# Optimization experiments

Measured on AMD Instinct MI355X. Metric: run time of the kernel, lower is better.

## Reference

```python
import jax, jax.numpy as jnp
import numpy as np

N, E = 50000, 800000
IN_C, OUT_C, H, EW_DIM = 64, 32, 4, 16
NEG_SLOPE = 0.2


def setup_inputs() -> dict:
    key = jax.random.key(0)
    ks = jax.random.split(key, 10)
    x = jax.random.normal(ks[0], (N, IN_C), dtype=jnp.float32)
    src = jax.random.randint(ks[1], (E,), 0, N)
    dst = jax.random.randint(ks[2], (E,), 0, N)
    edge_index = jnp.stack([src, dst]).astype(jnp.int64)
    edge_weight = jax.random.normal(ks[3], (E, EW_DIM), dtype=jnp.float32)
    # GATConv params: lin weight [IN_C, H*OUT_C], bias [H*OUT_C], att_src/att_dst [H, OUT_C]
    s = 1.0 / np.sqrt(IN_C)
    W = jax.random.uniform(ks[4], (IN_C, H * OUT_C), minval=-s, maxval=s, dtype=jnp.float32)
    b = jnp.zeros((H * OUT_C,), dtype=jnp.float32)
    att_src = jax.random.normal(ks[5], (H, OUT_C), dtype=jnp.float32) * 0.1
    att_dst = jax.random.normal(ks[6], (H, OUT_C), dtype=jnp.float32) * 0.1
    # edge_weight_lin params: [EW_DIM, H], [H]
    se = 1.0 / np.sqrt(EW_DIM)
    Wl = jax.random.uniform(ks[7], (EW_DIM, H), minval=-se, maxval=se, dtype=jnp.float32)
    bl = jax.random.uniform(ks[8], (H,), minval=-se, maxval=se, dtype=jnp.float32)
    return {"x": x, "edge_index": edge_index, "edge_weight": edge_weight,
            "W": W, "b": b, "att_src": att_src, "att_dst": att_dst,
            "Wl": Wl, "bl": bl}


def gate_forward(x, edge_index, edge_weight, W, b, att_src, att_dst, Wl, bl):
    n = x.shape[0]
    h = (x @ W).reshape(n, H, OUT_C)                      # [N,H,C]
    a_src = jnp.einsum('nhc,hc->nh', h, att_src)          # [N,H]
    a_dst = jnp.einsum('nhc,hc->nh', h, att_dst)          # [N,H]
    # per-edge attention logits from edge weights (softmax over heads)
    edge_alpha = jax.nn.softmax(edge_weight @ Wl + bl, axis=1)  # [E,H]
    # add self loops (GATConv default add_self_loops=True, fill_value='mean')
    loop = jnp.arange(n)
    src = jnp.concatenate([edge_index[0], loop])
    dst = jnp.concatenate([edge_index[1], loop])
    loop_alpha = jnp.broadcast_to(edge_alpha.mean(axis=0), (n, H))
    ea = jnp.concatenate([edge_alpha, loop_alpha], axis=0)      # [E+N,H]
    # per-edge logits: gather src/dst contributions + edge term
    alpha = jax.nn.leaky_relu(a_src[src] + a_dst[dst] + ea, NEG_SLOPE)  # [E+N,H]
    # segment softmax grouped by destination node
    amax = jax.ops.segment_max(alpha, dst, num_segments=n)
    ex = jnp.exp(alpha - amax[dst])
    denom = jax.ops.segment_sum(ex, dst, num_segments=n)
    alpha = ex / (denom[dst] + 1e-16)                     # [E+N,H]
    # weighted messages, scatter-add aggregate
    msg = h[src] * alpha[:, :, None]                      # [E+N,H,C]
    out = jax.ops.segment_sum(msg, dst, num_segments=n)   # [N,H,C]
    return out.reshape(n, H * OUT_C) + b


def reference(x, edge_index, edge_weight, W, b, att_src, att_dst, Wl, bl):
    return gate_forward(x, edge_index, edge_weight, W, b, att_src, att_dst, Wl, bl)
```

## Files before the change

### kernel.cpp

```cpp
#include <hip/hip_runtime.h>
#include <math.h>

#define IN_C 64
#define HC 128
#define NHEAD 4
#define EWD 16
#define NEG 0.2f

__device__ __forceinline__ float lrelu(float v) { return v > 0.f ? v : NEG * v; }
__device__ __forceinline__ unsigned short f2b(float f) {
    unsigned int u = __float_as_uint(f);
    unsigned int r = ((u >> 16) & 1u) + 0x7fffu;
    return (unsigned short)((u + r) >> 16);
}
__device__ __forceinline__ float b2f(unsigned int lo16) {
    return __uint_as_float(lo16 << 16);
}

__global__ void k_feat(const float* __restrict__ x, const float* __restrict__ W,
                       const float* __restrict__ att_s, const float* __restrict__ att_d,
                       unsigned short* __restrict__ h_bf, float* __restrict__ a_src,
                       float* __restrict__ a_dst, int N) {
    __shared__ float Ws[IN_C * HC];
    __shared__ float xs[4][IN_C];
    const int tid = threadIdx.x;
    {
        const float4* W4 = (const float4*)W;
        float4* Ws4 = (float4*)Ws;
#pragma unroll
        for (int i = 0; i < (IN_C * HC / 4) / 128; ++i)
            Ws4[tid + i * 128] = W4[tid + i * 128];
    }
    const float as = att_s[tid];
    const float ad = att_d[tid];
    const int head = tid >> 5;
    for (int base = blockIdx.x * 4; base < N; base += gridDim.x * 4) {
        const int nrows = min(4, N - base);
        __syncthreads();
        if (tid < 64) {
            int r = tid >> 4, q = tid & 15;
            if (r < nrows)
                ((float4*)&xs[r][0])[q] = ((const float4*)(x + (size_t)(base + r) * IN_C))[q];
        }
        __syncthreads();
        for (int r = 0; r < nrows; ++r) {
            float acc = 0.f;
#pragma unroll
            for (int c = 0; c < IN_C; ++c)
                acc = fmaf(xs[r][c], Ws[c * HC + tid], acc);
            const int n = base + r;
            h_bf[(size_t)n * HC + tid] = f2b(acc);
            float ps = acc * as, pd = acc * ad;
#pragma unroll
            for (int off = 16; off; off >>= 1) {
                ps += __shfl_xor(ps, off, 32);
                pd += __shfl_xor(pd, off, 32);
            }
            if ((tid & 31) == 0) {
                a_src[n * NHEAD + head] = ps;
                a_dst[n * NHEAD + head] = pd;
            }
        }
    }
}

__global__ void k_count(const int* __restrict__ dst, int* __restrict__ deg, int E) {
    int e = blockIdx.x * 256 + threadIdx.x;
    if (e < E) atomicAdd(&deg[dst[e]], 1);
}

__global__ void k_scan1(const int* __restrict__ deg, int* __restrict__ part, int N) {
    const int b = blockIdx.x, tid = threadIdx.x;
    int base = b * 1024 + tid * 4;
    int s = 0;
#pragma unroll
    for (int k = 0; k < 4; ++k) { int i = base + k; if (i < N) s += deg[i]; }
#pragma unroll
    for (int off = 32; off; off >>= 1) s += __shfl_xor(s, off, 64);
    __shared__ int ls[4];
    if ((tid & 63) == 0) ls[tid >> 6] = s;
    __syncthreads();
    if (tid == 0) part[b] = ls[0] + ls[1] + ls[2] + ls[3];
}

__global__ void k_scan2(int* part, int nb) {
    const int tid = threadIdx.x;
    int orig = (tid < nb) ? part[tid] : 0;
    int v = orig;
#pragma unroll
    for (int off = 1; off < 64; off <<= 1) {
        int t = __shfl_up(v, off, 64);
        if (tid >= off) v += t;
    }
    if (tid < nb) part[tid] = v - orig;
}

__global__ void k_scan3(const int* __restrict__ deg, const int* __restrict__ part,
                        int* __restrict__ rowptr, int* __restrict__ cursor, int N, int E) {
    const int b = blockIdx.x, tid = threadIdx.x;
    int base = b * 1024 + tid * 4;
    int d[4]; int s = 0;
#pragma unroll
    for (int k = 0; k < 4; ++k) { int i = base + k; d[k] = (i < N) ? deg[i] : 0; s += d[k]; }
    int v = s;
#pragma unroll
    for (int off = 1; off < 64; off <<= 1) {
        int t = __shfl_up(v, off, 64);
        if ((tid & 63) >= off) v += t;
    }
    __shared__ int wsum[4];
    if ((tid & 63) == 63) wsum[tid >> 6] = v;
    __syncthreads();
    int waveoff = 0;
    const int w = tid >> 6;
    for (int k = 0; k < w; ++k) waveoff += wsum[k];
    int excl = v - s + waveoff + part[b];
#pragma unroll
    for (int k = 0; k < 4; ++k) {
        int i = base + k;
        if (i < N) { rowptr[i] = excl; cursor[i] = excl; }
        excl += d[k];
    }
    if (b == 0 && tid == 0) rowptr[N] = E;
}

__global__ void k_fill(const int* __restrict__ src, const int* __restrict__ dst,
                       const float* __restrict__ ew, const float* __restrict__ Wl,
                       const float* __restrict__ bl,
                       const float* __restrict__ a_src, const float* __restrict__ a_dst,
                       int* __restrict__ cursor, uint4* __restrict__ csr,
                       float* __restrict__ partial, int E) {
    __shared__ float sW[EWD * NHEAD];
    __shared__ float sb[NHEAD];
    __shared__ float sred[4][4];
    const int tid = threadIdx.x;
    if (tid < EWD * NHEAD) sW[tid] = Wl[tid];
    if (tid < NHEAD) sb[tid] = bl[tid];
    __syncthreads();
    float loc[4] = {0.f, 0.f, 0.f, 0.f};
    const int e = blockIdx.x * 256 + tid;
    if (e < E) {
        const float4* w4 = (const float4*)(ew + (size_t)e * EWD);
        float v[4];
#pragma unroll
        for (int hh = 0; hh < 4; ++hh) v[hh] = sb[hh];
#pragma unroll
        for (int q = 0; q < 4; ++q) {
            float4 t = w4[q];
            float tv[4] = {t.x, t.y, t.z, t.w};
#pragma unroll
            for (int k = 0; k < 4; ++k)
#pragma unroll
                for (int hh = 0; hh < 4; ++hh)
                    v[hh] = fmaf(tv[k], sW[(q * 4 + k) * 4 + hh], v[hh]);
        }
        float m = fmaxf(fmaxf(v[0], v[1]), fmaxf(v[2], v[3]));
        float s = 0.f;
#pragma unroll
        for (int hh = 0; hh < 4; ++hh) { v[hh] = __expf(v[hh] - m); s += v[hh]; }
        float inv = 1.f / s;
#pragma unroll
        for (int hh = 0; hh < 4; ++hh) { v[hh] *= inv; loc[hh] += v[hh]; }
        const int sn = src[e], dn = dst[e];
        float4 as = ((const float4*)a_src)[sn];
        float4 ad = ((const float4*)a_dst)[dn];
        unsigned int e0 = f2b(__expf(lrelu(as.x + ad.x + v[0])));
        unsigned int e1 = f2b(__expf(lrelu(as.y + ad.y + v[1])));
        unsigned int e2 = f2b(__expf(lrelu(as.z + ad.z + v[2])));
        unsigned int e3 = f2b(__expf(lrelu(as.w + ad.w + v[3])));
        uint4 rec;
        rec.x = (unsigned int)sn;
        rec.y = e0 | (e1 << 16);
        rec.z = e2 | (e3 << 16);
        rec.w = 0u;
        int slot = atomicAdd(&cursor[dn], 1);
        csr[slot] = rec;
    }
    const int w = tid >> 6;
#pragma unroll
    for (int hh = 0; hh < 4; ++hh) {
        float v = loc[hh];
#pragma unroll
        for (int off = 32; off; off >>= 1) v += __shfl_xor(v, off, 64);
        if ((tid & 63) == 0) sred[w][hh] = v;
    }
    __syncthreads();
    if (tid < 4)
        partial[blockIdx.x * 4 + tid] =
            sred[0][tid] + sred[1][tid] + sred[2][tid] + sred[3][tid];
}

__global__ void k_red(const float* __restrict__ partial, float* __restrict__ asum, int nb) {
    const int tid = threadIdx.x;
    const int w = tid >> 6, lane = tid & 63;
    float s = 0.f;
    for (int b = lane; b < nb; b += 64) s += partial[b * 4 + w];
#pragma unroll
    for (int off = 32; off; off >>= 1) s += __shfl_xor(s, off, 64);
    if (lane == 0) asum[w] = s;
}

__global__ void k_agg(const unsigned short* __restrict__ h_bf, const int* __restrict__ rowptr,
                      const uint4* __restrict__ csr,
                      const float* __restrict__ a_src, const float* __restrict__ a_dst,
                      const float* __restrict__ asum, const float* __restrict__ bias,
                      float* __restrict__ out, int N, int E) {
    const int d = blockIdx.x;
    const int tid = threadIdx.x;
    const int head = tid >> 5;
    __shared__ int ssrc[32];
    __shared__ float sex[32][4];
    const int r0 = rowptr[d], r1 = rowptr[d + 1];
    float acc = 0.f, den = 0.f;
    for (int base = r0; base < r1; base += 32) {
        const int cnt = min(32, r1 - base);
        __syncthreads();
        if (tid < cnt) {
            uint4 rec = csr[base + tid];
            ssrc[tid] = (int)rec.x;
            sex[tid][0] = b2f(rec.y & 0xffffu);
            sex[tid][1] = b2f(rec.y >> 16);
            sex[tid][2] = b2f(rec.z & 0xffffu);
            sex[tid][3] = b2f(rec.z >> 16);
        }
        __syncthreads();
        int k = 0;
        for (; k + 4 <= cnt; k += 4) {
            const int s0 = ssrc[k], s1 = ssrc[k+1], s2 = ssrc[k+2], s3 = ssrc[k+3];
            const float e0 = sex[k][head], e1 = sex[k+1][head],
                        e2 = sex[k+2][head], e3 = sex[k+3][head];
            const float h0 = b2f(h_bf[(size_t)s0 * HC + tid]);
            const float h1 = b2f(h_bf[(size_t)s1 * HC + tid]);
            const float h2 = b2f(h_bf[(size_t)s2 * HC + tid]);
            const float h3 = b2f(h_bf[(size_t)s3 * HC + tid]);
            acc = fmaf(h0, e0, acc); den += e0;
            acc = fmaf(h1, e1, acc); den += e1;
            acc = fmaf(h2, e2, acc); den += e2;
            acc = fmaf(h3, e3, acc); den += e3;
        }
        for (; k < cnt; ++k) {
            const int s = ssrc[k];
            const float ex = sex[k][head];
            acc = fmaf(b2f(h_bf[(size_t)s * HC + tid]), ex, acc);
            den += ex;
        }
    }
    const float mean = asum[head] * (1.0f / (float)E);
    float l = lrelu(a_src[d * NHEAD + head] + a_dst[d * NHEAD + head] + mean);
    const float exl = __expf(l);
    acc = fmaf(b2f(h_bf[(size_t)d * HC + tid]), exl, acc);
    den += exl;
    out[(size_t)d * HC + tid] = acc / (den + 1e-16f) + bias[tid];
}

extern "C" void kernel_launch(void* const* d_in, const int* in_sizes, int n_in,
                              void* d_out, int out_size, void* d_ws, size_t ws_size,
                              hipStream_t stream) {
    const float* x     = (const float*)d_in[0];
    const int*   ei    = (const int*)d_in[1];
    const float* ew    = (const float*)d_in[2];
    const float* W     = (const float*)d_in[3];
    const float* bias  = (const float*)d_in[4];
    const float* att_s = (const float*)d_in[5];
    const float* att_d = (const float*)d_in[6];
    const float* Wl    = (const float*)d_in[7];
    const float* bl    = (const float*)d_in[8];
    const int N = in_sizes[0] / IN_C;
    const int E = in_sizes[1] / 2;
    const int* src = ei;
    const int* dst = ei + E;
    float* out = (float*)d_out;

    const int FILL_BLOCKS = (E + 255) / 256;

    float* ws = (float*)d_ws;
    size_t off = 0;
    unsigned short* h_bf = (unsigned short*)(ws + off); off += (size_t)N * HC / 2;
    float* a_src  = ws + off; off += (size_t)N * NHEAD;
    float* a_dst  = ws + off; off += (size_t)N * NHEAD;
    int*   deg    = (int*)(ws + off); off += N;
    float* asum   = ws + off; off += 4;
    int*   part   = (int*)(ws + off); off += 64;
    int*   rowptr = (int*)(ws + off); off += (size_t)N + 4;
    int*   cursor = (int*)(ws + off); off += N;
    uint4* csr    = (uint4*)(ws + off); off += (size_t)E * 4;
    float* partial= ws + off; off += (size_t)FILL_BLOCKS * 4;

    hipMemsetAsync(deg, 0, (size_t)N * 4, stream);

    k_feat<<<2048, 128, 0, stream>>>(x, W, att_s, att_d, h_bf, a_src, a_dst, N);
    k_count<<<(E + 255) / 256, 256, 0, stream>>>(dst, deg, E);
    const int nb = (N + 1023) / 1024;
    k_scan1<<<nb, 256, 0, stream>>>(deg, part, N);
    k_scan2<<<1, 64, 0, stream>>>(part, nb);
    k_scan3<<<nb, 256, 0, stream>>>(deg, part, rowptr, cursor, N, E);
    k_fill<<<FILL_BLOCKS, 256, 0, stream>>>(src, dst, ew, Wl, bl, a_src, a_dst,
                                            cursor, csr, partial, E);
    k_red<<<1, 256, 0, stream>>>(partial, asum, FILL_BLOCKS);
    k_agg<<<N, 128, 0, stream>>>(h_bf, rowptr, csr, a_src, a_dst,
                                 asum, bias, out, N, E);
}
```

Before: 300.8 us.

## Register-block feature GEMM, batch edges per thread, drop LDS staging in aggregation

k_feat now keeps W columns in registers and computes 8 rows per iteration instead of streaming W from shared memory row by row. k_count and k_fill each handle four edges per thread, issuing their gathers and atomics in batches to raise memory-level parallelism. k_agg reads CSR records directly from global memory, with no shared staging or barriers. The risks are higher register pressure from the 64-float wreg array and redundant per-thread CSR loads in k_agg.

```diff
diff --git a/kernel.cpp b/kernel.cpp
--- a/kernel.cpp
+++ b/kernel.cpp
@@ -16,57 +16,76 @@
 __device__ __forceinline__ float b2f(unsigned int lo16) {
     return __uint_as_float(lo16 << 16);
 }
+__device__ __forceinline__ float pickex(uint4 rec, int head) {
+    unsigned int pair = (head & 2) ? rec.z : rec.y;
+    unsigned int bits = (head & 1) ? (pair >> 16) : (pair & 0xffffu);
+    return b2f(bits);
+}
 
 __global__ void k_feat(const float* __restrict__ x, const float* __restrict__ W,
                        const float* __restrict__ att_s, const float* __restrict__ att_d,
                        unsigned short* __restrict__ h_bf, float* __restrict__ a_src,
                        float* __restrict__ a_dst, int N) {
-    __shared__ float Ws[IN_C * HC];
-    __shared__ float xs[4][IN_C];
-    const int tid = threadIdx.x;
-    {
-        const float4* W4 = (const float4*)W;
-        float4* Ws4 = (float4*)Ws;
-#pragma unroll
-        for (int i = 0; i < (IN_C * HC / 4) / 128; ++i)
-            Ws4[tid + i * 128] = W4[tid + i * 128];
-    }
+    __shared__ float xs[8][IN_C];
+    const int tid = threadIdx.x;
+    float wreg[IN_C];
+#pragma unroll
+    for (int k = 0; k < IN_C; ++k) wreg[k] = W[k * HC + tid];
     const float as = att_s[tid];
     const float ad = att_d[tid];
     const int head = tid >> 5;
-    for (int base = blockIdx.x * 4; base < N; base += gridDim.x * 4) {
-        const int nrows = min(4, N - base);
+    for (int base = blockIdx.x * 8; base < N; base += gridDim.x * 8) {
+        const int nrows = min(8, N - base);
         __syncthreads();
-        if (tid < 64) {
+        {
             int r = tid >> 4, q = tid & 15;
             if (r < nrows)
                 ((float4*)&xs[r][0])[q] = ((const float4*)(x + (size_t)(base + r) * IN_C))[q];
         }
         __syncthreads();
-        for (int r = 0; r < nrows; ++r) {
-            float acc = 0.f;
-#pragma unroll
-            for (int c = 0; c < IN_C; ++c)
-                acc = fmaf(xs[r][c], Ws[c * HC + tid], acc);
+        float acc[8] = {0.f, 0.f, 0.f, 0.f, 0.f, 0.f, 0.f, 0.f};
+#pragma unroll
+        for (int q = 0; q < 16; ++q) {
+#pragma unroll
+            for (int r = 0; r < 8; ++r) {
+                float4 xv = ((const float4*)&xs[r][0])[q];
+                acc[r] = fmaf(xv.x, wreg[4 * q + 0], acc[r]);
+                acc[r] = fmaf(xv.y, wreg[4 * q + 1], acc[r]);
+                acc[r] = fmaf(xv.z, wreg[4 * q + 2], acc[r]);
+                acc[r] = fmaf(xv.w, wreg[4 * q + 3], acc[r]);
+            }
+        }
+#pragma unroll
+        for (int r = 0; r < 8; ++r) {
             const int n = base + r;
-            h_bf[(size_t)n * HC + tid] = f2b(acc);
-            float ps = acc * as, pd = acc * ad;
-#pragma unroll
-            for (int off = 16; off; off >>= 1) {
-                ps += __shfl_xor(ps, off, 32);
-                pd += __shfl_xor(pd, off, 32);
+            if (r < nrows) {
+                h_bf[(size_t)n * HC + tid] = f2b(acc[r]);
+                float ps = acc[r] * as, pd = acc[r] * ad;
+#pragma unroll
+                for (int off = 16; off; off >>= 1) {
+                    ps += __shfl_xor(ps, off, 32);
+                    pd += __shfl_xor(pd, off, 32);
+                }
+                if ((tid & 31) == 0) {
+                    a_src[n * NHEAD + head] = ps;
+                    a_dst[n * NHEAD + head] = pd;
+                }
             }
-            if ((tid & 31) == 0) {
-                a_src[n * NHEAD + head] = ps;
-                a_dst[n * NHEAD + head] = pd;
-            }
         }
     }
 }
 
 __global__ void k_count(const int* __restrict__ dst, int* __restrict__ deg, int E) {
-    int e = blockIdx.x * 256 + threadIdx.x;
-    if (e < E) atomicAdd(&deg[dst[e]], 1);
+    const int ebase = blockIdx.x * 1024 + threadIdx.x;
+    int d[4];
+#pragma unroll
+    for (int i = 0; i < 4; ++i) {
+        int e = ebase + i * 256;
+        d[i] = (e < E) ? dst[e] : -1;
+    }
+#pragma unroll
+    for (int i = 0; i < 4; ++i)
+        if (d[i] >= 0) atomicAdd(&deg[d[i]], 1);
 }
 
 __global__ void k_scan1(const int* __restrict__ deg, int* __restrict__ part, int N) {
@@ -137,10 +156,28 @@
     if (tid < EWD * NHEAD) sW[tid] = Wl[tid];
     if (tid < NHEAD) sb[tid] = bl[tid];
     __syncthreads();
+    const int ebase = blockIdx.x * 1024 + tid;
+    bool val[4]; int sn[4], dn[4];
+#pragma unroll
+    for (int i = 0; i < 4; ++i) {
+        int e = ebase + i * 256;
+        val[i] = e < E;
+        int ec = val[i] ? e : 0;
+        sn[i] = src[ec];
+        dn[i] = dst[ec];
+    }
+    float4 as4[4], ad4[4];
+#pragma unroll
+    for (int i = 0; i < 4; ++i) {
+        as4[i] = ((const float4*)a_src)[sn[i]];
+        ad4[i] = ((const float4*)a_dst)[dn[i]];
+    }
     float loc[4] = {0.f, 0.f, 0.f, 0.f};
-    const int e = blockIdx.x * 256 + tid;
-    if (e < E) {
-        const float4* w4 = (const float4*)(ew + (size_t)e * EWD);
+    unsigned int recy[4], recz[4];
+#pragma unroll
+    for (int i = 0; i < 4; ++i) {
+        int ec = val[i] ? (ebase + i * 256) : 0;
+        const float4* w4 = (const float4*)(ew + (size_t)ec * EWD);
         float v[4];
 #pragma unroll
         for (int hh = 0; hh < 4; ++hh) v[hh] = sb[hh];
@@ -160,21 +197,31 @@
         for (int hh = 0; hh < 4; ++hh) { v[hh] = __expf(v[hh] - m); s += v[hh]; }
         float inv = 1.f / s;
 #pragma unroll
-        for (int hh = 0; hh < 4; ++hh) { v[hh] *= inv; loc[hh] += v[hh]; }
-        const int sn = src[e], dn = dst[e];
-        float4 as = ((const float4*)a_src)[sn];
-        float4 ad = ((const float4*)a_dst)[dn];
-        unsigned int e0 = f2b(__expf(lrelu(as.x + ad.x + v[0])));
-        unsigned int e1 = f2b(__expf(lrelu(as.y + ad.y + v[1])));
-        unsigned int e2 = f2b(__expf(lrelu(as.z + ad.z + v[2])));
-        unsigned int e3 = f2b(__expf(lrelu(as.w + ad.w + v[3])));
-        uint4 rec;
-        rec.x = (unsigned int)sn;
-        rec.y = e0 | (e1 << 16);
-        rec.z = e2 | (e3 << 16);
-        rec.w = 0u;
-        int slot = atomicAdd(&cursor[dn], 1);
-        csr[slot] = rec;
+        for (int hh = 0; hh < 4; ++hh) {
+            v[hh] *= inv;
+            if (val[i]) loc[hh] += v[hh];
+        }
+        unsigned int e0 = f2b(__expf(lrelu(as4[i].x + ad4[i].x + v[0])));
+        unsigned int e1 = f2b(__expf(lrelu(as4[i].y + ad4[i].y + v[1])));
+        unsigned int e2 = f2b(__expf(lrelu(as4[i].z + ad4[i].z + v[2])));
+        unsigned int e3 = f2b(__expf(lrelu(as4[i].w + ad4[i].w + v[3])));
+        recy[i] = e0 | (e1 << 16);
+        recz[i] = e2 | (e3 << 16);
+    }
+    int slot[4];
+#pragma unroll
+    for (int i = 0; i < 4; ++i)
+        slot[i] = val[i] ? atomicAdd(&cursor[dn[i]], 1) : 0;
+#pragma unroll
+    for (int i = 0; i < 4; ++i) {
+        if (val[i]) {
+            uint4 rec;
+            rec.x = (unsigned int)sn[i];
+            rec.y = recy[i];
+            rec.z = recz[i];
+            rec.w = 0u;
+            csr[slot[i]] = rec;
+        }
     }
     const int w = tid >> 6;
 #pragma unroll
@@ -208,42 +255,27 @@
     const int d = blockIdx.x;
     const int tid = threadIdx.x;
     const int head = tid >> 5;
-    __shared__ int ssrc[32];
-    __shared__ float sex[32][4];
     const int r0 = rowptr[d], r1 = rowptr[d + 1];
     float acc = 0.f, den = 0.f;
-    for (int base = r0; base < r1; base += 32) {
-        const int cnt = min(32, r1 - base);
-        __syncthreads();
-        if (tid < cnt) {
-            uint4 rec = csr[base + tid];
-            ssrc[tid] = (int)rec.x;
-            sex[tid][0] = b2f(rec.y & 0xffffu);
-            sex[tid][1] = b2f(rec.y >> 16);
-            sex[tid][2] = b2f(rec.z & 0xffffu);
-            sex[tid][3] = b2f(rec.z >> 16);
-        }
-        __syncthreads();
-        int k = 0;
-        for (; k + 4 <= cnt; k += 4) {
-            const int s0 = ssrc[k], s1 = ssrc[k+1], s2 = ssrc[k+2], s3 = ssrc[k+3];
-            const float e0 = sex[k][head], e1 = sex[k+1][head],
-                        e2 = sex[k+2][head], e3 = sex[k+3][head];
-            const float h0 = b2f(h_bf[(size_t)s0 * HC + tid]);
-            const float h1 = b2f(h_bf[(size_t)s1 * HC + tid]);
-            const float h2 = b2f(h_bf[(size_t)s2 * HC + tid]);
-            const float h3 = b2f(h_bf[(size_t)s3 * HC + tid]);
-            acc = fmaf(h0, e0, acc); den += e0;
-            acc = fmaf(h1, e1, acc); den += e1;
-            acc = fmaf(h2, e2, acc); den += e2;
-            acc = fmaf(h3, e3, acc); den += e3;
-        }
-        for (; k < cnt; ++k) {
-            const int s = ssrc[k];
-            const float ex = sex[k][head];
-            acc = fmaf(b2f(h_bf[(size_t)s * HC + tid]), ex, acc);
-            den += ex;
-        }
+    int k = r0;
+    for (; k + 4 <= r1; k += 4) {
+        const uint4 rA = csr[k], rB = csr[k + 1], rC = csr[k + 2], rD = csr[k + 3];
+        const float hA = b2f(h_bf[(size_t)rA.x * HC + tid]);
+        const float hB = b2f(h_bf[(size_t)rB.x * HC + tid]);
+        const float hC = b2f(h_bf[(size_t)rC.x * HC + tid]);
+        const float hD = b2f(h_bf[(size_t)rD.x * HC + tid]);
+        const float eA = pickex(rA, head), eB = pickex(rB, head);
+        const float eC = pickex(rC, head), eD = pickex(rD, head);
+        acc = fmaf(hA, eA, acc); den += eA;
+        acc = fmaf(hB, eB, acc); den += eB;
+        acc = fmaf(hC, eC, acc); den += eC;
+        acc = fmaf(hD, eD, acc); den += eD;
+    }
+    for (; k < r1; ++k) {
+        const uint4 rec = csr[k];
+        const float hv = b2f(h_bf[(size_t)rec.x * HC + tid]);
+        const float ev = pickex(rec, head);
+        acc = fmaf(hv, ev, acc); den += ev;
     }
     const float mean = asum[head] * (1.0f / (float)E);
     float l = lrelu(a_src[d * NHEAD + head] + a_dst[d * NHEAD + head] + mean);
@@ -271,7 +303,7 @@
     const int* dst = ei + E;
     float* out = (float*)d_out;
 
-    const int FILL_BLOCKS = (E + 255) / 256;
+    const int FILL_BLOCKS = (E + 1023) / 1024;
 
     float* ws = (float*)d_ws;
     size_t off = 0;
@@ -289,7 +321,7 @@
     hipMemsetAsync(deg, 0, (size_t)N * 4, stream);
 
     k_feat<<<2048, 128, 0, stream>>>(x, W, att_s, att_d, h_bf, a_src, a_dst, N);
-    k_count<<<(E + 255) / 256, 256, 0, stream>>>(dst, deg, E);
+    k_count<<<FILL_BLOCKS, 256, 0, stream>>>(dst, deg, E);
     const int nb = (N + 1023) / 1024;
     k_scan1<<<nb, 256, 0, stream>>>(deg, part, N);
     k_scan2<<<1, 64, 0, stream>>>(part, nb);
```

Result: slower. 911.0 us (+202.8%).
